# Performance work log

Hardware: AMD Instinct MI355X
Metric: run time of the kernel (lower is better)

## Reference

```python
import jax, jax.numpy as jnp
import numpy as np

N_LAYERS = 2        # f_aux_layer_num
DIM = 512           # aux_dim
HEADS = 8           # aux_attn_num
HEAD = DIM // HEADS # 64 == aux_attn_dim
FFN_H = int(DIM * 2.0)  # ffn_factor = 2.0 -> 1024
BLOCK = 64          # f_block_size n
L_BLOCKS = 32
M = BLOCK + 1       # block + router token
EPS = 1e-5
THETA = 10000.0


def rms_norm(x, w):
    return x * jax.lax.rsqrt(jnp.mean(x * x, axis=-1, keepdims=True) + EPS) * w


def rotary(x):
    # x: [b, h, s, a]; matches RotaryEmb: halves rotated with outer(t, inv_freq)
    s, a = x.shape[2], x.shape[3]
    inv_freq = (1.0 / THETA) ** (jnp.arange(0, a, 2, dtype=jnp.float32) / a)
    freqs = jnp.arange(s, dtype=jnp.float32)[:, None] * inv_freq[None, :]  # [s, a/2]
    cos, sin = jnp.cos(freqs), jnp.sin(freqs)
    x1, x2 = jnp.split(x, 2, axis=-1)
    return jnp.concatenate([x1 * cos + x2 * sin, -x1 * sin + x2 * cos], axis=-1)


def setup_inputs() -> dict:
    key = jax.random.key(0)
    ks = jax.random.split(key, 10)
    B = 2
    S = L_BLOCKS * M
    x = jax.random.normal(ks[0], (B, L_BLOCKS * BLOCK, DIM), jnp.float32)
    doc = jnp.sort(jax.random.randint(ks[1], (B, S), 0, 4, dtype=jnp.int32), axis=-1)
    w = 0.02
    return {
        "x": x,
        "doc": doc,
        "router_token": jax.random.normal(ks[2], (DIM,), jnp.float32),
        "attn_w": jax.random.normal(ks[3], (N_LAYERS, DIM, 3 * DIM), jnp.float32) * w,
        "attn_o_w": jax.random.normal(ks[4], (N_LAYERS, DIM, DIM), jnp.float32) * w,
        "ffn_up_w": jax.random.normal(ks[5], (N_LAYERS, DIM, 2 * FFN_H), jnp.float32) * w,
        "ffn_down_w": jax.random.normal(ks[6], (N_LAYERS, FFN_H, DIM), jnp.float32) * w,
        "attn_norm_w": jnp.ones((N_LAYERS, DIM), jnp.float32),
        "ffn_norm_w": jnp.ones((N_LAYERS, DIM), jnp.float32),
    }


def reference(x, doc, router_token, attn_w, attn_o_w, ffn_up_w, ffn_down_w,
              attn_norm_w, ffn_norm_w):
    b = x.shape[0]
    # insert router token after each block: [b, l, n+1, d] -> [b, s, d]
    xb = x.reshape(b, L_BLOCKS, BLOCK, DIM)
    rt = jnp.broadcast_to(router_token, (b, L_BLOCKS, 1, DIM))
    h = jnp.concatenate([xb, rt], axis=2).reshape(b, L_BLOCKS * M, DIM)
    s = h.shape[1]

    # mask_mod_1: block-causal AND same-doc
    blk = jnp.arange(s) // M
    causal = blk[:, None] >= blk[None, :]                       # [s, s]
    mask = causal[None] & (doc[:, :, None] == doc[:, None, :])  # [b, s, s]
    neg = jnp.finfo(h.dtype).min
    scale = 1.0 / jnp.sqrt(jnp.float32(HEAD))

    def split_heads(t):
        return t.reshape(b, s, HEADS, HEAD).transpose(0, 2, 1, 3)

    for i in range(N_LAYERS):
        hn = rms_norm(h, attn_norm_w[i])
        qkv = hn @ attn_w[i]                       # [b, s, 3*dim]
        q, k, v = jnp.split(qkv, 3, axis=-1)
        q, k, v = split_heads(q), split_heads(k), split_heads(v)
        q, k = rotary(q), rotary(k)
        scores = jnp.einsum('bhqa,bhka->bhqk', q, k) * scale
        scores = jnp.where(mask[:, None], scores, neg)
        attn = jax.nn.softmax(scores, axis=-1)
        o = jnp.einsum('bhqk,bhka->bhqa', attn, v)
        o = o.transpose(0, 2, 1, 3).reshape(b, s, DIM)
        h = h + o @ attn_o_w[i]
        hf = rms_norm(h, ffn_norm_w[i])
        u1, u2 = jnp.split(hf @ ffn_up_w[i], 2, axis=-1)
        h = h + (jax.nn.silu(u1) * u2) @ ffn_down_w[i]

    # keep router-token slot of each block: [b, l, d]
    return h.reshape(b, L_BLOCKS, M, DIM)[:, :, -1]
```

## Files before the change

### kernel.cpp

```cpp
#include <hip/hip_runtime.h>
#include <math.h>

#define NB 2
#define LB 32
#define BLKN 64
#define MM 65
#define SS (LB*MM)
#define DD 512
#define NH 8
#define HD 64
#define FFH 1024
#define ROWS (NB*SS)
#define WT_LS 2621440

typedef __attribute__((ext_vector_type(8))) short bf16x8;
typedef __attribute__((ext_vector_type(4))) float f32x4;

__device__ __forceinline__ unsigned short f2bf(float f) {
    union { float f; unsigned u; } v; v.f = f;
    unsigned r = (v.u + 0x7FFFu + ((v.u >> 16) & 1u)) >> 16;
    return (unsigned short)r;
}
__device__ __forceinline__ float bf2f(unsigned short u) {
    union { unsigned u; float f; } v; v.u = ((unsigned)u) << 16; return v.f;
}

__device__ __forceinline__ void gload_lds16(const unsigned short* g, unsigned short* l) {
    __builtin_amdgcn_global_load_lds((const __attribute__((address_space(1))) unsigned int*)g,
                                     (__attribute__((address_space(3))) unsigned int*)l,
                                     16, 0, 0);
}

__device__ __forceinline__ int grow_map(int r) {
    return (r >> 5) * SS + (r & 31) * MM + BLKN;
}

template <int FIRST>
__global__ __launch_bounds__(256) void rms4_k(const unsigned short* __restrict__ hsrc,
                                              const float* __restrict__ x,
                                              const float* __restrict__ rt,
                                              const float* __restrict__ w,
                                              unsigned short* __restrict__ hout,
                                              unsigned short* __restrict__ out) {
    int row = blockIdx.x * 4 + (threadIdx.x >> 6);
    int lane = threadIdx.x & 63;
    float v[8];
    if (FIRST) {
        int s = row % SS, b = row / SS;
        int l = s / MM, j = s % MM;
        const float* sp = (j < BLKN) ? x + ((size_t)(b * LB + l) * BLKN + j) * DD : rt;
        float4 a = *(const float4*)(sp + lane * 8);
        float4 bq = *(const float4*)(sp + lane * 8 + 4);
        v[0] = a.x; v[1] = a.y; v[2] = a.z; v[3] = a.w;
        v[4] = bq.x; v[5] = bq.y; v[6] = bq.z; v[7] = bq.w;
    } else {
        bf16x8 h8 = *(const bf16x8*)(hsrc + (size_t)row * DD + lane * 8);
        #pragma unroll
        for (int j = 0; j < 8; ++j) v[j] = bf2f((unsigned short)h8[j]);
    }
    float ss = 0.0f;
    #pragma unroll
    for (int j = 0; j < 8; ++j) ss += v[j] * v[j];
    #pragma unroll
    for (int off = 32; off; off >>= 1) ss += __shfl_xor(ss, off);
    float r = rsqrtf(ss * (1.0f / 512.0f) + 1e-5f);
    float4 w0 = *(const float4*)(w + lane * 8);
    float4 w1 = *(const float4*)(w + lane * 8 + 4);
    float wv[8] = {w0.x, w0.y, w0.z, w0.w, w1.x, w1.y, w1.z, w1.w};
    unsigned short o8[8];
    #pragma unroll
    for (int j = 0; j < 8; ++j) o8[j] = f2bf(v[j] * r * wv[j]);
    *(bf16x8*)(out + (size_t)row * DD + lane * 8) = *(const bf16x8*)o8;
    if (FIRST) {
        unsigned short h8[8];
        #pragma unroll
        for (int j = 0; j < 8; ++j) h8[j] = f2bf(v[j]);
        *(bf16x8*)(hout + (size_t)row * DD + lane * 8) = *(const bf16x8*)h8;
    }
}

__global__ __launch_bounds__(256) void wtrans_all_k(const float* __restrict__ attn_w,
                                                    const float* __restrict__ attn_o_w,
                                                    const float* __restrict__ up_w,
                                                    const float* __restrict__ down_w,
                                                    unsigned short* __restrict__ wt) {
    __shared__ unsigned short T[64][66];
    int wg = blockIdx.x;
    int layer = wg >= 640;
    int r = wg - layer * 640;
    const float* W; int K, N; size_t dstOff; int perm = 0;
    if (r < 192)      { W = attn_w   + (size_t)layer * 512 * 1536; K = 512;  N = 1536; dstOff = 0; }
    else if (r < 256) { W = attn_o_w + (size_t)layer * 512 * 512;  K = 512;  N = 512;  dstOff = 786432;  r -= 192; }
    else if (r < 512) { W = up_w     + (size_t)layer * 512 * 2048; K = 512;  N = 2048; dstOff = 1048576; perm = 1; r -= 256; }
    else              { W = down_w   + (size_t)layer * 1024 * 512; K = 1024; N = 512;  dstOff = 2097152; r -= 512; }
    unsigned short* dst = wt + (size_t)layer * WT_LS + dstOff;
    int ntn = N >> 6;
    int n0 = (r % ntn) * 64, k0 = (r / ntn) * 64;
    int t = threadIdx.x;
    #pragma unroll
    for (int i = 0; i < 16; ++i) {
        int e = t + i * 256;
        int rr = e >> 6, cc = e & 63;
        T[rr][cc] = f2bf(W[(size_t)(k0 + rr) * N + n0 + cc]);
    }
    __syncthreads();
    #pragma unroll
    for (int i = 0; i < 16; ++i) {
        int e = t + i * 256;
        int rr = e >> 6, cc = e & 63;
        int n = n0 + rr;
        int nr = n;
        if (perm) {
            int p = n & 1023;
            nr = ((p >> 4) << 5) | ((n >> 10) << 4) | (p & 15);
        }
        dst[(size_t)nr * K + k0 + cc] = T[cc][rr];
    }
}

template <int ADD, int OBF, int ROPE, int SILU>
__global__ __launch_bounds__(256) void gemm128_k(const unsigned short* __restrict__ A,
                                                 const unsigned short* __restrict__ Wt,
                                                 void* __restrict__ Cp,
                                                 int K, int N, int colOff) {
    __shared__ unsigned short As[128 * 64];
    __shared__ unsigned short Bs[128 * 64];
    int t = threadIdx.x;
    int lane = t & 63, wv = t >> 6;
    int wm = wv >> 1, wn = wv & 1;
    int rowBase = blockIdx.y * 128, colBase = blockIdx.x * 128;
    int c = lane & 15, g = lane >> 4;
    int sw = (c & 7) << 4;

    f32x4 acc[4][4];
    #pragma unroll
    for (int mt = 0; mt < 4; ++mt)
        #pragma unroll
        for (int nt = 0; nt < 4; ++nt) { f32x4 z = {0, 0, 0, 0}; acc[mt][nt] = z; }

    for (int k0 = 0; k0 < K; k0 += 64) {
        __syncthreads();
        #pragma unroll
        for (int i = 0; i < 4; ++i) {
            int e0 = (i * 4 + wv) * 64;
            int e = e0 + lane;
            int row = e >> 3;
            int kb = ((e & 7) << 4) ^ ((row & 7) << 4);
            int gr = rowBase + row; if (gr > ROWS - 1) gr = ROWS - 1;
            gload_lds16(A + (size_t)gr * K + k0 + (kb >> 1), &As[e0 * 8]);
        }
        #pragma unroll
        for (int i = 0; i < 4; ++i) {
            int e0 = (i * 4 + wv) * 64;
            int e = e0 + lane;
            int row = e >> 3;
            int kb = ((e & 7) << 4) ^ ((row & 7) << 4);
            gload_lds16(Wt + (size_t)(colOff + colBase + row) * K + k0 + (kb >> 1), &Bs[e0 * 8]);
        }
        __syncthreads();

        bf16x8 af[4][2], bfr[4][2];
        #pragma unroll
        for (int mt = 0; mt < 4; ++mt)
            #pragma unroll
            for (int hf = 0; hf < 2; ++hf)
                af[mt][hf] = *(const bf16x8*)
                    &As[((wm * 64 + mt * 16 + c) * 128 + ((hf * 64 + g * 16) ^ sw)) >> 1];
        #pragma unroll
        for (int nt = 0; nt < 4; ++nt)
            #pragma unroll
            for (int hf = 0; hf < 2; ++hf)
                bfr[nt][hf] = *(const bf16x8*)
                    &Bs[((wn * 64 + nt * 16 + c) * 128 + ((hf * 64 + g * 16) ^ sw)) >> 1];
        __builtin_amdgcn_s_setprio(1);
        #pragma unroll
        for (int mt = 0; mt < 4; ++mt)
            #pragma unroll
            for (int nt = 0; nt < 4; ++nt) {
                acc[mt][nt] = __builtin_amdgcn_mfma_f32_16x16x32_bf16(af[mt][0], bfr[nt][0], acc[mt][nt], 0, 0, 0);
                acc[mt][nt] = __builtin_amdgcn_mfma_f32_16x16x32_bf16(af[mt][1], bfr[nt][1], acc[mt][nt], 0, 0, 0);
            }
        __builtin_amdgcn_s_setprio(0);
    }

    if (ROPE) {
        int sec = (colOff + colBase + wn * 64) >> 9;
        if (sec < 2) {
            #pragma unroll
            for (int mt = 0; mt < 4; ++mt)
                #pragma unroll
                for (int j = 0; j < 4; ++j) {
                    int row = rowBase + wm * 64 + mt * 16 + g * 4 + j;
                    int spos = row % SS;
                    #pragma unroll
                    for (int p = 0; p < 2; ++p) {
                        float jj = (float)(c + p * 16);
                        float inv = exp2f(jj * -0.41524101186092030f);
                        float fr = (float)spos * inv;
                        float sn, cs; __sincosf(fr, &sn, &cs);
                        float a = acc[mt][p][j], bb = acc[mt][p + 2][j];
                        acc[mt][p][j] = a * cs + bb * sn;
                        acc[mt][p + 2][j] = -a * sn + bb * cs;
                    }
                }
        }
    }

    #pragma unroll
    for (int mt = 0; mt < 4; ++mt)
        #pragma unroll
        for (int j = 0; j < 4; ++j) {
            int row = rowBase + wm * 64 + mt * 16 + g * 4 + j;
            if (row >= ROWS) continue;
            if (SILU) {
                unsigned short* gr = (unsigned short*)Cp + (size_t)row * 1024;
                #pragma unroll
                for (int ntp = 0; ntp < 2; ++ntp) {
                    int npr = colBase + wn * 64 + ntp * 32;
                    int p = ((npr >> 5) << 4) + c;
                    float u1 = acc[mt][2 * ntp][j];
                    float u2 = acc[mt][2 * ntp + 1][j];
                    gr[p] = f2bf((u1 / (1.0f + __expf(-u1))) * u2);
                }
            } else {
                size_t off = (size_t)row * N + colOff + colBase + wn * 64 + c;
                if (OBF) {
                    unsigned short* cr = (unsigned short*)Cp + off;
                    #pragma unroll
                    for (int nt = 0; nt < 4; ++nt) cr[nt * 16] = f2bf(acc[mt][nt][j]);
                } else {
                    float* cr = (float*)Cp + off;
                    #pragma unroll
                    for (int nt = 0; nt < 4; ++nt) {
                        if (ADD) cr[nt * 16] += acc[mt][nt][j];
                        else     cr[nt * 16] = acc[mt][nt][j];
                    }
                }
            }
        }
}

template <int MODE, int ADD>
__global__ __launch_bounds__(256) void gemm64_k(const unsigned short* __restrict__ A,
                                                const unsigned short* __restrict__ Wt,
                                                void* __restrict__ Cp,
                                                const unsigned short* __restrict__ Hsrc,
                                                float* __restrict__ outp,
                                                int K, int N) {
    __shared__ unsigned short As[64 * 64];
    __shared__ unsigned short Bs[128 * 64];
    int t = threadIdx.x;
    int lane = t & 63, wv = t >> 6;
    int wm = wv >> 1, wn = wv & 1;
    int rowBase = blockIdx.y * 64, colBase = blockIdx.x * 128;
    int c = lane & 15, g = lane >> 4;
    int sw = (c & 7) << 4;

    f32x4 acc[2][4];
    #pragma unroll
    for (int mt = 0; mt < 2; ++mt)
        #pragma unroll
        for (int nt = 0; nt < 4; ++nt) { f32x4 z = {0, 0, 0, 0}; acc[mt][nt] = z; }

    for (int k0 = 0; k0 < K; k0 += 64) {
        __syncthreads();
        #pragma unroll
        for (int i = 0; i < 2; ++i) {
            int e0 = (i * 4 + wv) * 64;
            int e = e0 + lane;
            int row = e >> 3;
            int kb = ((e & 7) << 4) ^ ((row & 7) << 4);
            int gr = rowBase + row;
            gload_lds16(A + (size_t)gr * K + k0 + (kb >> 1), &As[e0 * 8]);
        }
        #pragma unroll
        for (int i = 0; i < 4; ++i) {
            int e0 = (i * 4 + wv) * 64;
            int e = e0 + lane;
            int row = e >> 3;
            int kb = ((e & 7) << 4) ^ ((row & 7) << 4);
            gload_lds16(Wt + (size_t)(colBase + row) * K + k0 + (kb >> 1), &Bs[e0 * 8]);
        }
        __syncthreads();

        bf16x8 af[2][2], bfr[4][2];
        #pragma unroll
        for (int mt = 0; mt < 2; ++mt)
            #pragma unroll
            for (int hf = 0; hf < 2; ++hf)
                af[mt][hf] = *(const bf16x8*)
                    &As[((wm * 32 + mt * 16 + c) * 128 + ((hf * 64 + g * 16) ^ sw)) >> 1];
        #pragma unroll
        for (int nt = 0; nt < 4; ++nt)
            #pragma unroll
            for (int hf = 0; hf < 2; ++hf)
                bfr[nt][hf] = *(const bf16x8*)
                    &Bs[((wn * 64 + nt * 16 + c) * 128 + ((hf * 64 + g * 16) ^ sw)) >> 1];
        __builtin_amdgcn_s_setprio(1);
        #pragma unroll
        for (int mt = 0; mt < 2; ++mt)
            #pragma unroll
            for (int nt = 0; nt < 4; ++nt) {
                acc[mt][nt] = __builtin_amdgcn_mfma_f32_16x16x32_bf16(af[mt][0], bfr[nt][0], acc[mt][nt], 0, 0, 0);
                acc[mt][nt] = __builtin_amdgcn_mfma_f32_16x16x32_bf16(af[mt][1], bfr[nt][1], acc[mt][nt], 0, 0, 0);
            }
        __builtin_amdgcn_s_setprio(0);
    }

    #pragma unroll
    for (int mt = 0; mt < 2; ++mt)
        #pragma unroll
        for (int j = 0; j < 4; ++j) {
            int row = rowBase + wm * 32 + mt * 16 + g * 4 + j;
            int col = colBase + wn * 64 + c;
            if (MODE == 0) {
                if (ADD) {
                    unsigned short* cr = (unsigned short*)Cp + (size_t)row * N + col;
                    #pragma unroll
                    for (int nt = 0; nt < 4; ++nt)
                        cr[nt * 16] = f2bf(bf2f(cr[nt * 16]) + acc[mt][nt][j]);
                } else {
                    float* cr = (float*)Cp + (size_t)row * N + col;
                    #pragma unroll
                    for (int nt = 0; nt < 4; ++nt) cr[nt * 16] = acc[mt][nt][j];
                }
            } else if (MODE == 2) {
                int gr = grow_map(row);
                unsigned short* cr = (unsigned short*)Cp + (size_t)row * 512 + col;
                const unsigned short* hsr = Hsrc + (size_t)gr * 512 + col;
                #pragma unroll
                for (int nt = 0; nt < 4; ++nt)
                    cr[nt * 16] = f2bf(bf2f(hsr[nt * 16]) + acc[mt][nt][j]);
            } else if (MODE == 3) {
                float* cr = outp + (size_t)row * 512 + col;
                const unsigned short* hsr = Hsrc + (size_t)row * 512 + col;
                #pragma unroll
                for (int nt = 0; nt < 4; ++nt) cr[nt * 16] = bf2f(hsr[nt * 16]) + acc[mt][nt][j];
            } else {
                unsigned short* gr = (unsigned short*)Cp + (size_t)row * 1024;
                #pragma unroll
                for (int ntp = 0; ntp < 2; ++ntp) {
                    int npr = colBase + wn * 64 + ntp * 32;
                    int p = ((npr >> 5) << 4) + c;
                    float u1 = acc[mt][2 * ntp][j];
                    float u2 = acc[mt][2 * ntp + 1][j];
                    gr[p] = f2bf((u1 / (1.0f + __expf(-u1))) * u2);
                }
            }
        }
}

#define QR 80

__global__ __launch_bounds__(320) void attn_mfma_k(const unsigned short* __restrict__ qkv,
                                                   const int* __restrict__ doc,
                                                   unsigned short* __restrict__ o) {
    __shared__ unsigned short QP[5760];
    __shared__ unsigned short Ks[2][64 * 64];
    __shared__ unsigned short Vt[2][64][72];
    __shared__ int docq[QR];
    __shared__ int dock[2][64];

    unsigned short* Qs = QP;
    unsigned short (*Ps)[16][72] = (unsigned short (*)[16][72])QP;

    int idx = blockIdx.x;
    int l = (idx < 256) ? (31 - (idx >> 4)) : ((idx - 256) >> 4);
    int b = (idx >> 3) & 1;
    int h = idx & 7;
    int t = threadIdx.x;
    int lane = t & 63;
    int wv = t >> 6;

    const unsigned short* qb = qkv + (size_t)b * SS * 1536;
    int rowq0 = l * MM;
    int kmax = (l + 1) * MM;

    #pragma unroll
    for (int it = 0; it < 2; ++it) {
        int ebase = it * 320 + wv * 64;
        int e = ebase + lane;
        int row = e >> 3;
        int kb = ((e & 7) << 4) ^ ((row & 7) << 4);
        int gr = rowq0 + row; if (gr > SS - 1) gr = SS - 1;
        gload_lds16(qb + (size_t)gr * 1536 + h * 64 + (kb >> 1), &Qs[ebase * 8]);
    }
    if (t < QR) docq[t] = (t < MM) ? doc[b * SS + rowq0 + t] : -999999;

    int d0 = doc[b * SS + rowq0];
    int lo = 0, hi = rowq0;
    while (lo < hi) {
        int mid = (lo + hi) >> 1;
        if (doc[b * SS + mid] < d0) lo = mid + 1; else hi = mid;
    }
    int kts = lo >> 6;
    int nkt = (kmax + 63) >> 6;

    const int mt = wv;
    const int g = lane >> 4;
    const int c = lane & 15;
    const int sw = (c & 7) << 4;

    auto stageK = [&](int kbase, int buf) {
        int ebase = wv * 64;
        int e = ebase + lane;
        int row = e >> 3;
        int kb = ((e & 7) << 4) ^ ((row & 7) << 4);
        int kg = kbase + row; if (kg > kmax - 1) kg = kmax - 1;
        gload_lds16(qb + (size_t)kg * 1536 + 512 + h * 64 + (kb >> 1), &Ks[buf][ebase * 8]);
        if (wv < 3) {
            int eb2 = 320 + wv * 64;
            int e2 = eb2 + lane;
            int row2 = e2 >> 3;
            int kb2 = ((e2 & 7) << 4) ^ ((row2 & 7) << 4);
            int kg2 = kbase + row2; if (kg2 > kmax - 1) kg2 = kmax - 1;
            gload_lds16(qb + (size_t)kg2 * 1536 + 512 + h * 64 + (kb2 >> 1), &Ks[buf][eb2 * 8]);
        }
    };
    bf16x8 vr0, vr1; int dnx = 0;
    auto loadV = [&](int kbase) {
        int key = t & 63;
        int de = (t >> 6) * 8;
        int kg = kbase + key; if (kg > kmax - 1) kg = kmax - 1;
        vr0 = *(const bf16x8*)(qb + (size_t)kg * 1536 + 1024 + h * 64 + de);
        if (t < 192) {
            int e2 = 320 + t;
            int key2 = e2 & 63;
            int de2 = (e2 >> 6) * 8;
            int kg2 = kbase + key2; if (kg2 > kmax - 1) kg2 = kmax - 1;
            vr1 = *(const bf16x8*)(qb + (size_t)kg2 * 1536 + 1024 + h * 64 + de2);
        }
        if (t < 64) dnx = (kbase + t < kmax) ? doc[b * SS + kbase + t] : -1000000;
    };
    auto writeV = [&](int buf) {
        int key = t & 63;
        int de = (t >> 6) * 8;
        #pragma unroll
        for (int jj = 0; jj < 8; ++jj) Vt[buf][de + jj][key] = ((unsigned short*)&vr0)[jj];
        if (t < 192) {
            int e2 = 320 + t;
            int key2 = e2 & 63;
            int de2 = (e2 >> 6) * 8;
            #pragma unroll
            for (int jj = 0; jj < 8; ++jj) Vt[buf][de2 + jj][key2] = ((unsigned short*)&vr1)[jj];
        }
        if (t < 64) dock[buf][t] = dnx;
    };

    stageK(kts << 6, 0);
    loadV(kts << 6);
    writeV(0);
    __syncthreads();

    bf16x8 aq[2];
    #pragma unroll
    for (int hf = 0; hf < 2; ++hf)
        aq[hf] = *(const bf16x8*)&Qs[((mt * 16 + c) * 128 + ((hf * 64 + g * 16) ^ sw)) >> 1];
    int dq[4];
    #pragma unroll
    for (int j = 0; j < 4; ++j) dq[j] = docq[mt * 16 + g * 4 + j];
    __syncthreads();

    f32x4 oacc[4];
    float m_[4], l_[4];
    #pragma unroll
    for (int nt = 0; nt < 4; ++nt) { f32x4 z = {0,0,0,0}; oacc[nt] = z; }
    #pragma unroll
    for (int j = 0; j < 4; ++j) { m_[j] = -1e30f; l_[j] = 0.0f; }

    for (int kt = kts; kt < nkt; ++kt) {
        int cur = (kt - kts) & 1;
        bool more = (kt + 1 < nkt);
        if (more) {
            stageK((kt + 1) << 6, cur ^ 1);
            loadV((kt + 1) << 6);
        }

        f32x4 s[4];
        __builtin_amdgcn_s_setprio(1);
        #pragma unroll
        for (int sub = 0; sub < 4; ++sub) {
            f32x4 acc = {0, 0, 0, 0};
            #pragma unroll
            for (int hf = 0; hf < 2; ++hf) {
                bf16x8 bk = *(const bf16x8*)
                    &Ks[cur][((sub * 16 + c) * 128 + ((hf * 64 + g * 16) ^ sw)) >> 1];
                acc = __builtin_amdgcn_mfma_f32_16x16x32_bf16(aq[hf], bk, acc, 0, 0, 0);
            }
            s[sub] = acc;
        }
        __builtin_amdgcn_s_setprio(0);
        #pragma unroll
        for (int sub = 0; sub < 4; ++sub) {
            int dk = dock[cur][sub * 16 + c];
            #pragma unroll
            for (int j = 0; j < 4; ++j)
                s[sub][j] = (dq[j] == dk) ? s[sub][j] * 0.125f : -1e30f;
        }
        float mx[4];
        #pragma unroll
        for (int j = 0; j < 4; ++j)
            mx[j] = fmaxf(fmaxf(s[0][j], s[1][j]), fmaxf(s[2][j], s[3][j]));
        #pragma unroll
        for (int off = 1; off < 16; off <<= 1)
            #pragma unroll
            for (int j = 0; j < 4; ++j) mx[j] = fmaxf(mx[j], __shfl_xor(mx[j], off));
        float mn[4], sc[4], rs[4];
        #pragma unroll
        for (int j = 0; j < 4; ++j) {
            mn[j] = fmaxf(m_[j], mx[j]);
            sc[j] = __expf(m_[j] - mn[j]);
            m_[j] = mn[j];
            rs[j] = 0.0f;
        }
        #pragma unroll
        for (int sub = 0; sub < 4; ++sub)
            #pragma unroll
            for (int j = 0; j < 4; ++j) {
                float p = __expf(s[sub][j] - mn[j]);
                rs[j] += p;
                Ps[wv][g * 4 + j][sub * 16 + c] = f2bf(p);
            }
        #pragma unroll
        for (int off = 1; off < 16; off <<= 1)
            #pragma unroll
            for (int j = 0; j < 4; ++j) rs[j] += __shfl_xor(rs[j], off);
        #pragma unroll
        for (int j = 0; j < 4; ++j) l_[j] = l_[j] * sc[j] + rs[j];
        #pragma unroll
        for (int nt = 0; nt < 4; ++nt)
            #pragma unroll
            for (int j = 0; j < 4; ++j) oacc[nt][j] *= sc[j];
        __builtin_amdgcn_s_setprio(1);
        #pragma unroll
        for (int hf = 0; hf < 2; ++hf) {
            bf16x8 af = *(const bf16x8*)&Ps[wv][c][hf * 32 + g * 8];
            #pragma unroll
            for (int nt = 0; nt < 4; ++nt) {
                bf16x8 bv = *(const bf16x8*)&Vt[cur][nt * 16 + c][hf * 32 + g * 8];
                oacc[nt] = __builtin_amdgcn_mfma_f32_16x16x32_bf16(af, bv, oacc[nt], 0, 0, 0);
            }
        }
        __builtin_amdgcn_s_setprio(0);

        if (more) writeV(cur ^ 1);
        __syncthreads();
    }

    #pragma unroll
    for (int j = 0; j < 4; ++j) {
        int row = mt * 16 + g * 4 + j;
        if (row < MM) {
            float invl = 1.0f / l_[j];
            #pragma unroll
            for (int nt = 0; nt < 4; ++nt)
                o[(size_t)(b * SS + rowq0 + row) * DD + h * 64 + nt * 16 + c] =
                    f2bf(oacc[nt][j] * invl);
        }
    }
}

__global__ __launch_bounds__(256) void rattn_k(const unsigned short* __restrict__ hnb,
                                               const unsigned short* __restrict__ qkv,
                                               const unsigned short* __restrict__ wq,
                                               const int* __restrict__ doc,
                                               unsigned short* __restrict__ obr) {
    __shared__ float hn_r[DD];
    __shared__ float qs[HD];
    __shared__ float sc[SS];
    __shared__ float red_m[4], red_s[4];
    __shared__ float pacc[4][HD];

    int idx = blockIdx.x;
    int b = idx >> 8, h = (idx >> 5) & 7, l = idx & 31;
    int t = threadIdx.x;
    int lane = t & 63, wv = t >> 6;

    const unsigned short* qb = qkv + (size_t)b * SS * 1536;
    int spos = l * MM + BLKN;
    int rowq = b * SS + spos;
    int kmax = (l + 1) * MM;

    {
        unsigned v = *(const unsigned*)(hnb + (size_t)rowq * DD + t * 2);
        hn_r[t * 2] = bf2f((unsigned short)(v & 0xffff));
        hn_r[t * 2 + 1] = bf2f((unsigned short)(v >> 16));
    }
    int dr = doc[rowq];
    int lo = 0, hi = spos;
    while (lo < hi) {
        int mid = (lo + hi) >> 1;
        if (doc[b * SS + mid] < dr) lo = mid + 1; else hi = mid;
    }
    __syncthreads();

    {
        float part = 0.0f;
        const unsigned short* wr = wq + (size_t)(h * 64 + lane) * DD + wv * 128;
        #pragma unroll
        for (int k8 = 0; k8 < 16; ++k8) {
            bf16x8 w8 = *(const bf16x8*)(wr + k8 * 8);
            #pragma unroll
            for (int j = 0; j < 8; ++j)
                part += hn_r[wv * 128 + k8 * 8 + j] * bf2f((unsigned short)w8[j]);
        }
        pacc[wv][lane] = part;
    }
    __syncthreads();
    if (wv == 0) {
        float dq = pacc[0][lane] + pacc[1][lane] + pacc[2][lane] + pacc[3][lane];
        float other = __shfl_xor(dq, 32);
        float jj = (float)(lane & 31);
        float inv = exp2f(jj * -0.41524101186092030f);
        float fr = (float)spos * inv;
        float sn, cs; __sincosf(fr, &sn, &cs);
        float q1 = (lane < 32) ? dq : other;
        float q2 = (lane < 32) ? other : dq;
        qs[lane] = (lane < 32) ? (q1 * cs + q2 * sn) : (-q1 * sn + q2 * cs);
    }
    __syncthreads();

    int dc = lane & 7, k8 = lane >> 3;
    float mx = -1e30f;
    for (int k0 = lo; k0 < kmax; k0 += 32) {
        int k = k0 + wv * 8 + k8;
        float d = 0.0f;
        if (k < kmax) {
            bf16x8 kv = *(const bf16x8*)(qb + (size_t)k * 1536 + 512 + h * 64 + dc * 8);
            #pragma unroll
            for (int j = 0; j < 8; ++j)
                d += bf2f((unsigned short)kv[j]) * qs[dc * 8 + j];
        }
        #pragma unroll
        for (int off = 1; off < 8; off <<= 1) d += __shfl_xor(d, off);
        if (k < kmax) {
            float s = d * 0.125f;
            if (dc == 0) sc[k] = s;
            mx = fmaxf(mx, s);
        }
    }
    #pragma unroll
    for (int off = 32; off; off >>= 1) mx = fmaxf(mx, __shfl_xor(mx, off));
    if (lane == 0) red_m[wv] = mx;
    __syncthreads();
    mx = fmaxf(fmaxf(red_m[0], red_m[1]), fmaxf(red_m[2], red_m[3]));

    float sum = 0.0f;
    for (int k = lo + t; k < kmax; k += 256) {
        float p = __expf(sc[k] - mx);
        sc[k] = p;
        sum += p;
    }
    #pragma unroll
    for (int off = 32; off; off >>= 1) sum += __shfl_xor(sum, off);
    if (lane == 0) red_s[wv] = sum;
    __syncthreads();
    sum = red_s[0] + red_s[1] + red_s[2] + red_s[3];

    float a0 = 0, a1 = 0, a2 = 0, a3 = 0;
    int k = lo + wv;
    for (; k + 12 < kmax; k += 16) {
        a0 += sc[k]      * bf2f(qb[(size_t)k * 1536 + 1024 + h * 64 + lane]);
        a1 += sc[k + 4]  * bf2f(qb[(size_t)(k + 4) * 1536 + 1024 + h * 64 + lane]);
        a2 += sc[k + 8]  * bf2f(qb[(size_t)(k + 8) * 1536 + 1024 + h * 64 + lane]);
        a3 += sc[k + 12] * bf2f(qb[(size_t)(k + 12) * 1536 + 1024 + h * 64 + lane]);
    }
    for (; k < kmax; k += 4)
        a0 += sc[k] * bf2f(qb[(size_t)k * 1536 + 1024 + h * 64 + lane]);
    pacc[wv][lane] = (a0 + a1) + (a2 + a3);
    __syncthreads();
    if (wv == 0) {
        float o = (pacc[0][lane] + pacc[1][lane] + pacc[2][lane] + pacc[3][lane]) / sum;
        obr[(size_t)(b * LB + l) * DD + h * 64 + lane] = f2bf(o);
    }
}

extern "C" void kernel_launch(void* const* d_in, const int* in_sizes, int n_in,
                              void* d_out, int out_size, void* d_ws, size_t ws_size,
                              hipStream_t stream) {
    const float* x           = (const float*)d_in[0];
    const int*   doc         = (const int*)d_in[1];
    const float* rt          = (const float*)d_in[2];
    const float* attn_w      = (const float*)d_in[3];
    const float* attn_o_w    = (const float*)d_in[4];
    const float* ffn_up_w    = (const float*)d_in[5];
    const float* ffn_down_w  = (const float*)d_in[6];
    const float* attn_norm_w = (const float*)d_in[7];
    const float* ffn_norm_w  = (const float*)d_in[8];
    float* out = (float*)d_out;

    unsigned short* hb   = (unsigned short*)d_ws;
    unsigned short* qkvb = hb + (size_t)ROWS * 512;
    unsigned short* wt   = qkvb + (size_t)ROWS * 1536;
    unsigned short* hnb  = wt + (size_t)2 * WT_LS;
    unsigned short* ob   = hnb + (size_t)ROWS * 512;
    unsigned short* gb   = ob + (size_t)ROWS * 512;
    unsigned short* obr  = gb + (size_t)ROWS * 1024;
    unsigned short* hnr  = obr + 64 * 512;
    unsigned short* gbr  = hnr + 64 * 512;
    unsigned short* hr   = gbr + 64 * 1024;

    wtrans_all_k<<<1280, 256, 0, stream>>>(attn_w, attn_o_w, ffn_up_w, ffn_down_w, wt);

    rms4_k<1><<<ROWS / 4, 256, 0, stream>>>(hb, x, rt, attn_norm_w, hb, hnb);
    gemm128_k<0, 1, 1, 0><<<dim3(12, 33), 256, 0, stream>>>(hnb, wt, qkvb, 512, 1536, 0);
    attn_mfma_k<<<512, 320, 0, stream>>>(qkvb, doc, ob);
    gemm64_k<0, 1><<<dim3(4, 65), 256, 0, stream>>>(ob, wt + 786432, hb, nullptr, nullptr, 512, 512);
    rms4_k<0><<<ROWS / 4, 256, 0, stream>>>(hb, x, rt, ffn_norm_w, nullptr, hnb);
    gemm128_k<0, 0, 0, 1><<<dim3(16, 33), 256, 0, stream>>>(hnb, wt + 1048576, gb, 512, 2048, 0);
    gemm64_k<0, 1><<<dim3(4, 65), 256, 0, stream>>>(gb, wt + 2097152, hb, nullptr, nullptr, 1024, 512);

    unsigned short* wl = wt + (size_t)WT_LS;
    rms4_k<0><<<ROWS / 4, 256, 0, stream>>>(hb, x, rt, attn_norm_w + 512, nullptr, hnb);
    gemm128_k<0, 1, 1, 0><<<dim3(8, 33), 256, 0, stream>>>(hnb, wl, qkvb, 512, 1536, 512);
    rattn_k<<<512, 256, 0, stream>>>(hnb, qkvb, wl, doc, obr);
    gemm64_k<2, 0><<<dim3(4, 1), 256, 0, stream>>>(obr, wl + 786432, hr, hb, nullptr, 512, 512);
    rms4_k<0><<<16, 256, 0, stream>>>(hr, x, rt, ffn_norm_w + 512, nullptr, hnr);
    gemm64_k<4, 0><<<dim3(16, 1), 256, 0, stream>>>(hnr, wl + 1048576, gbr, nullptr, nullptr, 512, 2048);
    gemm64_k<3, 0><<<dim3(4, 1), 256, 0, stream>>>(gbr, wl + 2097152, nullptr, hr, out, 1024, 512);
}
```

Baseline: 187.3 us.

## Emit V transposed from QKV GEMM epilogue and async-stage it in attention

The QKV GEMM epilogue now writes the V section into a separate head-major, sequence-contiguous buffer instead of the row-major qkv buffer. The attention kernel can then copy V tiles straight from global memory into swizzled LDS with async loads, replacing the register load plus scalar LDS transpose. The router-attention kernel also reads V from this buffer. The trade-off is scattered 2-byte stores in the GEMM epilogue, per-lane strided V reads in the router kernel, and extra workspace for the transposed copy.

```diff
diff --git a/kernel.cpp b/kernel.cpp
--- a/kernel.cpp
+++ b/kernel.cpp
@@ -122,6 +122,7 @@
 __global__ __launch_bounds__(256) void gemm128_k(const unsigned short* __restrict__ A,
                                                  const unsigned short* __restrict__ Wt,
                                                  void* __restrict__ Cp,
+                                                 unsigned short* __restrict__ vT,
                                                  int K, int N, int colOff) {
     __shared__ unsigned short As[128 * 64];
     __shared__ unsigned short Bs[128 * 64];
@@ -183,27 +184,25 @@
         __builtin_amdgcn_s_setprio(0);
     }
 
-    if (ROPE) {
-        int sec = (colOff + colBase + wn * 64) >> 9;
-        if (sec < 2) {
-            #pragma unroll
-            for (int mt = 0; mt < 4; ++mt)
+    int sec = ROPE ? ((colOff + colBase + wn * 64) >> 9) : 0;
+    if (ROPE && sec < 2) {
+        #pragma unroll
+        for (int mt = 0; mt < 4; ++mt)
+            #pragma unroll
+            for (int j = 0; j < 4; ++j) {
+                int row = rowBase + wm * 64 + mt * 16 + g * 4 + j;
+                int spos = row % SS;
                 #pragma unroll
-                for (int j = 0; j < 4; ++j) {
-                    int row = rowBase + wm * 64 + mt * 16 + g * 4 + j;
-                    int spos = row % SS;
-                    #pragma unroll
-                    for (int p = 0; p < 2; ++p) {
-                        float jj = (float)(c + p * 16);
-                        float inv = exp2f(jj * -0.41524101186092030f);
-                        float fr = (float)spos * inv;
-                        float sn, cs; __sincosf(fr, &sn, &cs);
-                        float a = acc[mt][p][j], bb = acc[mt][p + 2][j];
-                        acc[mt][p][j] = a * cs + bb * sn;
-                        acc[mt][p + 2][j] = -a * sn + bb * cs;
-                    }
+                for (int p = 0; p < 2; ++p) {
+                    float jj = (float)(c + p * 16);
+                    float inv = exp2f(jj * -0.41524101186092030f);
+                    float fr = (float)spos * inv;
+                    float sn, cs; __sincosf(fr, &sn, &cs);
+                    float a = acc[mt][p][j], bb = acc[mt][p + 2][j];
+                    acc[mt][p][j] = a * cs + bb * sn;
+                    acc[mt][p + 2][j] = -a * sn + bb * cs;
                 }
-        }
+            }
     }
 
     #pragma unroll
@@ -221,6 +220,13 @@
                     float u1 = acc[mt][2 * ntp][j];
                     float u2 = acc[mt][2 * ntp + 1][j];
                     gr[p] = f2bf((u1 / (1.0f + __expf(-u1))) * u2);
+                }
+            } else if (ROPE && sec == 2) {
+                int bb = row / SS, s = row % SS;
+                #pragma unroll
+                for (int nt = 0; nt < 4; ++nt) {
+                    int dg = colOff + colBase + wn * 64 + c + nt * 16 - 1024;
+                    vT[(size_t)(bb * 512 + dg) * SS + s] = f2bf(acc[mt][nt][j]);
                 }
             } else {
                 size_t off = (size_t)row * N + colOff + colBase + wn * 64 + c;
@@ -353,11 +359,12 @@
 #define QR 80
 
 __global__ __launch_bounds__(320) void attn_mfma_k(const unsigned short* __restrict__ qkv,
+                                                   const unsigned short* __restrict__ vT,
                                                    const int* __restrict__ doc,
                                                    unsigned short* __restrict__ o) {
     __shared__ unsigned short QP[5760];
     __shared__ unsigned short Ks[2][64 * 64];
-    __shared__ unsigned short Vt[2][64][72];
+    __shared__ unsigned short Vs[2][64 * 64];
     __shared__ int docq[QR];
     __shared__ int dock[2][64];
 
@@ -373,6 +380,7 @@
     int wv = t >> 6;
 
     const unsigned short* qb = qkv + (size_t)b * SS * 1536;
+    const unsigned short* vb = vT + (size_t)(b * 512 + h * 64) * SS;
     int rowq0 = l * MM;
     int kmax = (l + 1) * MM;
 
@@ -417,39 +425,27 @@
             gload_lds16(qb + (size_t)kg2 * 1536 + 512 + h * 64 + (kb2 >> 1), &Ks[buf][eb2 * 8]);
         }
     };
-    bf16x8 vr0, vr1; int dnx = 0;
-    auto loadV = [&](int kbase) {
-        int key = t & 63;
-        int de = (t >> 6) * 8;
-        int kg = kbase + key; if (kg > kmax - 1) kg = kmax - 1;
-        vr0 = *(const bf16x8*)(qb + (size_t)kg * 1536 + 1024 + h * 64 + de);
-        if (t < 192) {
-            int e2 = 320 + t;
-            int key2 = e2 & 63;
-            int de2 = (e2 >> 6) * 8;
-            int kg2 = kbase + key2; if (kg2 > kmax - 1) kg2 = kmax - 1;
-            vr1 = *(const bf16x8*)(qb + (size_t)kg2 * 1536 + 1024 + h * 64 + de2);
-        }
-        if (t < 64) dnx = (kbase + t < kmax) ? doc[b * SS + kbase + t] : -1000000;
+    auto stageV = [&](int kbase, int buf) {
+        int ebase = wv * 64;
+        int e = ebase + lane;
+        int d = e >> 3;
+        int kb = ((e & 7) << 4) ^ ((d & 7) << 4);
+        gload_lds16(vb + (size_t)d * SS + kbase + (kb >> 1), &Vs[buf][ebase * 8]);
+        if (wv < 3) {
+            int eb2 = 320 + wv * 64;
+            int e2 = eb2 + lane;
+            int d2 = e2 >> 3;
+            int kb2 = ((e2 & 7) << 4) ^ ((d2 & 7) << 4);
+            gload_lds16(vb + (size_t)d2 * SS + kbase + (kb2 >> 1), &Vs[buf][eb2 * 8]);
+        }
     };
-    auto writeV = [&](int buf) {
-        int key = t & 63;
-        int de = (t >> 6) * 8;
-        #pragma unroll
-        for (int jj = 0; jj < 8; ++jj) Vt[buf][de + jj][key] = ((unsigned short*)&vr0)[jj];
-        if (t < 192) {
-            int e2 = 320 + t;
-            int key2 = e2 & 63;
-            int de2 = (e2 >> 6) * 8;
-            #pragma unroll
-            for (int jj = 0; jj < 8; ++jj) Vt[buf][de2 + jj][key2] = ((unsigned short*)&vr1)[jj];
-        }
-        if (t < 64) dock[buf][t] = dnx;
-    };
 
     stageK(kts << 6, 0);
-    loadV(kts << 6);
-    writeV(0);
+    stageV(kts << 6, 0);
+    if (t < 64) {
+        int kg = (kts << 6) + t;
+        dock[0][t] = (kg < kmax) ? doc[b * SS + kg] : -1000000;
+    }
     __syncthreads();
 
     bf16x8 aq[2];
@@ -471,9 +467,14 @@
     for (int kt = kts; kt < nkt; ++kt) {
         int cur = (kt - kts) & 1;
         bool more = (kt + 1 < nkt);
+        int dnx = 0;
         if (more) {
             stageK((kt + 1) << 6, cur ^ 1);
-            loadV((kt + 1) << 6);
+            stageV((kt + 1) << 6, cur ^ 1);
+            if (t < 64) {
+                int kg = ((kt + 1) << 6) + t;
+                dnx = (kg < kmax) ? doc[b * SS + kg] : -1000000;
+            }
         }
 
         f32x4 s[4];
@@ -537,13 +538,14 @@
             bf16x8 af = *(const bf16x8*)&Ps[wv][c][hf * 32 + g * 8];
             #pragma unroll
             for (int nt = 0; nt < 4; ++nt) {
-                bf16x8 bv = *(const bf16x8*)&Vt[cur][nt * 16 + c][hf * 32 + g * 8];
+                bf16x8 bv = *(const bf16x8*)
+                    &Vs[cur][((nt * 16 + c) * 128 + ((hf * 64 + g * 16) ^ sw)) >> 1];
                 oacc[nt] = __builtin_amdgcn_mfma_f32_16x16x32_bf16(af, bv, oacc[nt], 0, 0, 0);
             }
         }
         __builtin_amdgcn_s_setprio(0);
 
-        if (more) writeV(cur ^ 1);
+        if (more && t < 64) dock[cur ^ 1][t] = dnx;
         __syncthreads();
     }
 
@@ -562,6 +564,7 @@
 
 __global__ __launch_bounds__(256) void rattn_k(const unsigned short* __restrict__ hnb,
                                                const unsigned short* __restrict__ qkv,
+                                               const unsigned short* __restrict__ vT,
                                                const unsigned short* __restrict__ wq,
                                                const int* __restrict__ doc,
                                                unsigned short* __restrict__ obr) {
@@ -577,6 +580,7 @@
     int lane = t & 63, wv = t >> 6;
 
     const unsigned short* qb = qkv + (size_t)b * SS * 1536;
+    const unsigned short* vrow = vT + (size_t)(b * 512 + h * 64 + lane) * SS;
     int spos = l * MM + BLKN;
     int rowq = b * SS + spos;
     int kmax = (l + 1) * MM;
@@ -660,13 +664,13 @@
     float a0 = 0, a1 = 0, a2 = 0, a3 = 0;
     int k = lo + wv;
     for (; k + 12 < kmax; k += 16) {
-        a0 += sc[k]      * bf2f(qb[(size_t)k * 1536 + 1024 + h * 64 + lane]);
-        a1 += sc[k + 4]  * bf2f(qb[(size_t)(k + 4) * 1536 + 1024 + h * 64 + lane]);
-        a2 += sc[k + 8]  * bf2f(qb[(size_t)(k + 8) * 1536 + 1024 + h * 64 + lane]);
-        a3 += sc[k + 12] * bf2f(qb[(size_t)(k + 12) * 1536 + 1024 + h * 64 + lane]);
+        a0 += sc[k]      * bf2f(vrow[k]);
+        a1 += sc[k + 4]  * bf2f(vrow[k + 4]);
+        a2 += sc[k + 8]  * bf2f(vrow[k + 8]);
+        a3 += sc[k + 12] * bf2f(vrow[k + 12]);
     }
     for (; k < kmax; k += 4)
-        a0 += sc[k] * bf2f(qb[(size_t)k * 1536 + 1024 + h * 64 + lane]);
+        a0 += sc[k] * bf2f(vrow[k]);
     pacc[wv][lane] = (a0 + a1) + (a2 + a3);
     __syncthreads();
     if (wv == 0) {
@@ -699,21 +703,22 @@
     unsigned short* hnr  = obr + 64 * 512;
     unsigned short* gbr  = hnr + 64 * 512;
     unsigned short* hr   = gbr + 64 * 1024;
+    unsigned short* vTb  = hr + 64 * 512;
 
     wtrans_all_k<<<1280, 256, 0, stream>>>(attn_w, attn_o_w, ffn_up_w, ffn_down_w, wt);
 
     rms4_k<1><<<ROWS / 4, 256, 0, stream>>>(hb, x, rt, attn_norm_w, hb, hnb);
-    gemm128_k<0, 1, 1, 0><<<dim3(12, 33), 256, 0, stream>>>(hnb, wt, qkvb, 512, 1536, 0);
-    attn_mfma_k<<<512, 320, 0, stream>>>(qkvb, doc, ob);
+    gemm128_k<0, 1, 1, 0><<<dim3(12, 33), 256, 0, stream>>>(hnb, wt, qkvb, vTb, 512, 1536, 0);
+    attn_mfma_k<<<512, 320, 0, stream>>>(qkvb, vTb, doc, ob);
     gemm64_k<0, 1><<<dim3(4, 65), 256, 0, stream>>>(ob, wt + 786432, hb, nullptr, nullptr, 512, 512);
     rms4_k<0><<<ROWS / 4, 256, 0, stream>>>(hb, x, rt, ffn_norm_w, nullptr, hnb);
-    gemm128_k<0, 0, 0, 1><<<dim3(16, 33), 256, 0, stream>>>(hnb, wt + 1048576, gb, 512, 2048, 0);
+    gemm128_k<0, 0, 0, 1><<<dim3(16, 33), 256, 0, stream>>>(hnb, wt + 1048576, gb, nullptr, 512, 2048, 0);
     gemm64_k<0, 1><<<dim3(4, 65), 256, 0, stream>>>(gb, wt + 2097152, hb, nullptr, nullptr, 1024, 512);
 
     unsigned short* wl = wt + (size_t)WT_LS;
     rms4_k<0><<<ROWS / 4, 256, 0, stream>>>(hb, x, rt, attn_norm_w + 512, nullptr, hnb);
-    gemm128_k<0, 1, 1, 0><<<dim3(8, 33), 256, 0, stream>>>(hnb, wl, qkvb, 512, 1536, 512);
-    rattn_k<<<512, 256, 0, stream>>>(hnb, qkvb, wl, doc, obr);
+    gemm128_k<0, 1, 1, 0><<<dim3(8, 33), 256, 0, stream>>>(hnb, wl, qkvb, vTb, 512, 1536, 512);
+    rattn_k<<<512, 256, 0, stream>>>(hnb, qkvb, vTb, wl, doc, obr);
     gemm64_k<2, 0><<<dim3(4, 1), 256, 0, stream>>>(obr, wl + 786432, hr, hb, nullptr, 512, 512);
     rms4_k<0><<<16, 256, 0, stream>>>(hr, x, rt, ffn_norm_w + 512, nullptr, hnr);
     gemm64_k<4, 0><<<dim3(16, 1), 256, 0, stream>>>(hnr, wl + 1048576, gbr, nullptr, nullptr, 512, 2048);
```

After: 215.4 us. +15.0%, slower.
